# Kernel tuning notes

Measured on AMD Instinct MI355X. Metric: run time of the kernel, lower is better.

The kernel has to match this reference:

```python
import jax, jax.numpy as jnp
import numpy as np

N_NODES = 50000
N_EDGES = 300000
N_GRAPHS = 2048
N_FEATS = 128
DIM_OUT = 32


def setup_inputs() -> dict:
    key = jax.random.key(0)
    ks = jax.random.split(key, 10)
    def glorot(k, shape):
        fan_in, fan_out = shape
        lim = (6.0 / (fan_in + fan_out)) ** 0.5
        return jax.random.uniform(k, shape, jnp.float32, -lim, lim)
    x = jax.random.normal(ks[0], (N_NODES, N_FEATS), jnp.float32)
    edge_index = jax.random.randint(ks[1], (2, N_EDGES), 0, N_NODES, jnp.int64)
    batch = jnp.sort(jax.random.randint(ks[2], (N_NODES,), 0, N_GRAPHS, jnp.int64))
    return {
        "x": x,
        "edge_index": edge_index,
        "batch": batch,
        "W1": glorot(ks[3], (N_FEATS, 256)), "b1": jnp.zeros((256,), jnp.float32),
        "W2": glorot(ks[4], (256, 256)),     "b2": jnp.zeros((256,), jnp.float32),
        "W3": glorot(ks[5], (256, 256)),     "b3": jnp.zeros((256,), jnp.float32),
        "Wf1": glorot(ks[6], (256, 128)),    "bf1": jnp.zeros((128,), jnp.float32),
        "Wf2": glorot(ks[7], (128, DIM_OUT)), "bf2": jnp.zeros((DIM_OUT,), jnp.float32),
    }


def _gcn_norm(edge_index, num_nodes):
    # PyG GCNConv default: add self-loops, symmetric D^-1/2 (A+I) D^-1/2 norm.
    loop = jnp.arange(num_nodes, dtype=edge_index.dtype)
    src = jnp.concatenate([edge_index[0], loop])
    dst = jnp.concatenate([edge_index[1], loop])
    deg = jax.ops.segment_sum(jnp.ones_like(dst, jnp.float32), dst, num_segments=num_nodes)
    dinv = jnp.where(deg > 0, deg ** -0.5, 0.0)
    norm = dinv[src] * dinv[dst]  # [E + N]
    return src, dst, norm


def _gcn_conv(x, src, dst, norm, W, b):
    h = x @ W                                # [N, C] transform first (efficient)
    msg = h[src] * norm[:, None]             # gather + scale, [E+N, C]
    agg = jax.ops.segment_sum(msg, dst, num_segments=x.shape[0])
    return agg + b


def reference(x, edge_index, batch, W1, b1, W2, b2, W3, b3, Wf1, bf1, Wf2, bf2):
    n = x.shape[0]
    src, dst, norm = _gcn_norm(edge_index, n)
    h = jax.nn.relu(_gcn_conv(x, src, dst, norm, W1, b1))
    h = jax.nn.relu(_gcn_conv(h, src, dst, norm, W2, b2))
    h = jax.nn.relu(_gcn_conv(h, src, dst, norm, W3, b3))
    # global_mean_pool over batch segment ids
    sums = jax.ops.segment_sum(h, batch, num_segments=N_GRAPHS)
    cnts = jax.ops.segment_sum(jnp.ones((n,), jnp.float32), batch, num_segments=N_GRAPHS)
    hg = sums / jnp.maximum(cnts, 1.0)[:, None]
    h = jax.nn.relu(hg @ Wf1 + bf1)
    return h @ Wf2 + bf2  # [N_GRAPHS, DIM_OUT]
```

## Files before the change

kernel.cpp:

```cpp
#include <hip/hip_runtime.h>
#include <hip/hip_bf16.h>

#define NNODES 50000
#define NEDGES 300000
#define NGRAPH 2048
#define NFEAT  128
#define NHID   256
#define DOUT   32
#define NROWS  50048

typedef __bf16 bf16x8 __attribute__((ext_vector_type(8)));
typedef float  f32x4  __attribute__((ext_vector_type(4)));
typedef int    i32x4  __attribute__((ext_vector_type(4)));
typedef unsigned short ushort8v __attribute__((ext_vector_type(8)));
typedef __attribute__((address_space(1))) const void* gas_ptr;
typedef __attribute__((address_space(3))) void* las_ptr;

__device__ __forceinline__ float bf2f(unsigned short u) {
    return __uint_as_float(((unsigned)u) << 16);
}
__device__ __forceinline__ unsigned short f2bf(float f) {
    unsigned u = __float_as_uint(f);
    unsigned r = u + 0x7FFFu + ((u >> 16) & 1u);
    return (unsigned short)(r >> 16);
}
__device__ __forceinline__ float sb2f(unsigned v, int k) {
    return (float)((signed char)(v >> (8 * k)));
}


template<int K>
__device__ __forceinline__ void wquant(const float* __restrict__ W, unsigned char* __restrict__ Wq,
                                       float* __restrict__ bsc, int t) {
    constexpr int EPR = K / 16;
    int n = t >> 4, p = t & 15;
    float vals[EPR];
    float mx = 0.f;
#pragma unroll
    for (int j = 0; j < EPR; ++j) {
        float v = W[(size_t)(p * EPR + j) * 256 + n];
        vals[j] = v;
        mx = fmaxf(mx, fabsf(v));
    }
    mx = fmaxf(mx, __shfl_xor(mx, 1, 16));
    mx = fmaxf(mx, __shfl_xor(mx, 2, 16));
    mx = fmaxf(mx, __shfl_xor(mx, 4, 16));
    mx = fmaxf(mx, __shfl_xor(mx, 8, 16));
    float inv = (mx > 0.f) ? 127.f / mx : 0.f;
#pragma unroll
    for (int j4 = 0; j4 < EPR / 4; ++j4) {
        unsigned pw = 0;
#pragma unroll
        for (int b = 0; b < 4; ++b) {
            int qv = (int)rintf(vals[j4 * 4 + b] * inv);
            pw |= ((unsigned)(qv & 255)) << (8 * b);
        }
        int k = p * EPR + j4 * 4;
        *(unsigned*)&Wq[(k >> 6) * 16384 + n * 64 + (k & 63)] = pw;
    }
    if (p == 0) bsc[n] = mx * (1.f / 127.f);
}

__global__ __launch_bounds__(256) void prep_k(const float* __restrict__ x, unsigned short* __restrict__ x16,
                                              const float* __restrict__ W1, const float* __restrict__ W2,
                                              const float* __restrict__ W3, const float* __restrict__ Wf1,
                                              const float* __restrict__ Wf2,
                                              unsigned char* __restrict__ Wq1, unsigned char* __restrict__ Wq2,
                                              unsigned char* __restrict__ Wq3,
                                              float* __restrict__ bsc1, float* __restrict__ bsc2,
                                              float* __restrict__ bsc3,
                                              unsigned short* __restrict__ Wf1t, unsigned short* __restrict__ Wf2t,
                                              int* __restrict__ cnt, int* __restrict__ fill,
                                              int4* __restrict__ adj8z) {
    int idx = blockIdx.x * 256 + threadIdx.x;
    if (idx < 800000) {
        int i = idx * 8;
        float4 a = *(const float4*)&x[i];
        float4 b = *(const float4*)&x[i + 4];
        ushort8v o = { f2bf(a.x), f2bf(a.y), f2bf(a.z), f2bf(a.w),
                       f2bf(b.x), f2bf(b.y), f2bf(b.z), f2bf(b.w) };
        int row = idx >> 4, ch = idx & 15;
        ((ushort8v*)x16)[(size_t)(row << 4) | (ch ^ (row & 7))] = o;
        return;
    }
    int t = idx - 800000;
    if (t < 4096)  { wquant<128>(W1, Wq1, bsc1, t); return; }
    t -= 4096;
    if (t < 4096)  { wquant<256>(W2, Wq2, bsc2, t); return; }
    t -= 4096;
    if (t < 4096)  { wquant<256>(W3, Wq3, bsc3, t); return; }
    t -= 4096;
    if (t < 36864) {
        const float* W; unsigned short* Wt; int K, N;
        if (t < 32768) { W = Wf1; Wt = Wf1t; K = 256; N = 128; }
        else           { W = Wf2; Wt = Wf2t; K = 128; N = 32; t -= 32768; }
        int n = t / K, k = t - n * K;
        Wt[t] = f2bf(W[(size_t)k * N + n]);
        return;
    }
    t -= 36864;
    if (t < NNODES) { cnt[t] = 0; fill[t] = 0; return; }
    t -= NNODES;
    if (t < 200000) { int4 z4 = {0, 0, 0, 0}; adj8z[t] = z4; }
}

__global__ __launch_bounds__(256) void edge_hist_k(const int* __restrict__ dst, int* cnt, int E) {
    int e = blockIdx.x * 256 + threadIdx.x;
    if (e < E) atomicAdd(&cnt[dst[e]], 1);
}

__global__ __launch_bounds__(1024) void scan_block_k(const int* __restrict__ cnt, int* __restrict__ rowp,
                                                     int* __restrict__ part, float* __restrict__ dinv,
                                                     int2* __restrict__ hdr, int n) {
    __shared__ int s[1024];
    int tid = threadIdx.x;
    int i = blockIdx.x * 1024 + tid;
    int v = (i < n) ? cnt[i] : 0;
    if (i < n) {
        float dv = rsqrtf((float)(v + 1));
        dinv[i] = dv;
        hdr[i] = make_int2(v, __float_as_int(dv * dv));
    }
    s[tid] = v;
    __syncthreads();
    for (int off = 1; off < 1024; off <<= 1) {
        int t = (tid >= off) ? s[tid - off] : 0;
        __syncthreads();
        s[tid] += t;
        __syncthreads();
    }
    if (i < n) rowp[i] = s[tid] - v;
    if (tid == 1023) part[blockIdx.x] = s[1023];
}

__global__ __launch_bounds__(256) void scatter_k(const int* __restrict__ src, const int* __restrict__ dst,
                                                 const int* __restrict__ rowp_pre, const int* __restrict__ part,
                                                 int* fill, const float* __restrict__ dinv,
                                                 int2* __restrict__ adj8, int2* __restrict__ adj,
                                                 int* __restrict__ rowp_fin,
                                                 const int* __restrict__ batch, int* __restrict__ gstart,
                                                 int E, int n, int nb) {
    __shared__ int s[64];
    int tid = threadIdx.x;
    if (tid < 64) s[tid] = (tid < nb) ? part[tid] : 0;
    __syncthreads();
    for (int off = 1; off < 64; off <<= 1) {
        int t = 0;
        if (tid < 64 && tid >= off) t = s[tid - off];
        __syncthreads();
        if (tid < 64) s[tid] += t;
        __syncthreads();
    }
    int gid = blockIdx.x * 256 + tid;
    if (gid <= n) {
        if (gid < n) {
            int ch = gid >> 10;
            int base = (ch == 0) ? 0 : s[ch - 1];
            rowp_fin[gid] = rowp_pre[gid] + base;
        } else {
            rowp_fin[n] = s[nb - 1];
        }
    }
    if (gid < n) {
        int b = batch[gid];
        int prev = (gid == 0) ? -1 : batch[gid - 1];
        for (int g = prev + 1; g <= b; ++g) gstart[g] = gid;
        if (gid == n - 1)
            for (int g = b + 1; g <= NGRAPH; ++g) gstart[g] = n;
    }
    if (gid < E) {
        int ss = src[gid], d = dst[gid];
        int f = atomicAdd(&fill[d], 1);
        int2 a; a.x = ss; a.y = __float_as_int(dinv[ss] * dinv[d]);
        if (f < 8) {
            adj8[d * 8 + f] = a;
        } else {
            int ch = d >> 10;
            int base = (ch == 0) ? 0 : s[ch - 1];
            adj[rowp_pre[d] + base + f] = a;
        }
    }
}

__global__ __launch_bounds__(256) void agg1_k(const unsigned short* __restrict__ T,
                                              const int4* __restrict__ adj8,
                                              const int2* __restrict__ hdr,
                                              const int* __restrict__ rowf,
                                              const int2* __restrict__ adj,
                                              unsigned char* __restrict__ z8,
                                              float* __restrict__ asc, int n) {
    int g  = threadIdx.x >> 4;
    int li = threadIdx.x & 15;
    int node = blockIdx.x * 16 + g;
    if (node >= n) return;
    const ushort8v* tp = (const ushort8v*)T;
    int2 h = hdr[node];
    int deg = h.x;
    float sw = __int_as_float(h.y);
    ushort8v u = tp[(size_t)node * 16 + (li ^ (node & 7))];
    int4 s4[4];
#pragma unroll
    for (int j = 0; j < 4; ++j) s4[j] = adj8[node * 4 + j];
    float ac[8];
#pragma unroll
    for (int k = 0; k < 8; ++k) ac[k] = bf2f(u[k]) * sw;
    int c[8]; float w[8];
#pragma unroll
    for (int j = 0; j < 4; ++j) {
        c[2 * j]     = s4[j].x; w[2 * j]     = __int_as_float(s4[j].y);
        c[2 * j + 1] = s4[j].z; w[2 * j + 1] = __int_as_float(s4[j].w);
    }
    ushort8v mm[8];
#pragma unroll
    for (int j = 0; j < 8; ++j) mm[j] = tp[(size_t)c[j] * 16 + (li ^ (c[j] & 7))];
#pragma unroll
    for (int j = 0; j < 8; ++j)
#pragma unroll
        for (int k = 0; k < 8; ++k)
            ac[k] += bf2f(mm[j][k]) * w[j];
    if (deg > 8) {
        int e0 = rowf[node], e1 = e0 + deg;
        for (int e = e0 + 8; e < e1; e += 4) {
            int2 a2[4];
#pragma unroll
            for (int j = 0; j < 4; ++j) {
                int ee = e + j;
                a2[j] = (ee < e1) ? adj[ee] : make_int2(0, 0);
            }
            ushort8v m2[4];
#pragma unroll
            for (int j = 0; j < 4; ++j) m2[j] = tp[(size_t)a2[j].x * 16 + (li ^ (a2[j].x & 7))];
#pragma unroll
            for (int j = 0; j < 4; ++j)
#pragma unroll
                for (int k = 0; k < 8; ++k)
                    ac[k] += bf2f(m2[j][k]) * __int_as_float(a2[j].y);
        }
    }
    float mx = 0.f;
#pragma unroll
    for (int k = 0; k < 8; ++k) mx = fmaxf(mx, fabsf(ac[k]));
    mx = fmaxf(mx, __shfl_xor(mx, 1, 16));
    mx = fmaxf(mx, __shfl_xor(mx, 2, 16));
    mx = fmaxf(mx, __shfl_xor(mx, 4, 16));
    mx = fmaxf(mx, __shfl_xor(mx, 8, 16));
    float inv = (mx > 0.f) ? 127.f / mx : 0.f;
    unsigned w0 = 0, w1 = 0;
#pragma unroll
    for (int k = 0; k < 4; ++k) {
        int q0 = (int)rintf(ac[k] * inv);
        int q1 = (int)rintf(ac[k + 4] * inv);
        w0 |= ((unsigned)(q0 & 255)) << (8 * k);
        w1 |= ((unsigned)(q1 & 255)) << (8 * k);
    }
    ((uint2*)z8)[(size_t)node * 16 + ((li >> 1) ^ (node & 7)) * 2 + (li & 1)] = make_uint2(w0, w1);
    if (li == 0) asc[node] = mx * (1.f / 127.f);
}

__global__ __launch_bounds__(256) void agg_q_k(const unsigned char* __restrict__ Hq,
                                               const float* __restrict__ csc,
                                               const int4* __restrict__ adj8,
                                               const int2* __restrict__ hdr,
                                               const int* __restrict__ rowf,
                                               const int2* __restrict__ adj,
                                               unsigned char* __restrict__ z8,
                                               float* __restrict__ asc, int n) {
    int g  = threadIdx.x >> 5;
    int li = threadIdx.x & 31;
    int node = blockIdx.x * 8 + g;
    if (node >= n) return;
    const uint2* qp = (const uint2*)Hq;
    int2 h = hdr[node];
    int deg = h.x;
    float swgt = __int_as_float(h.y) * csc[node];
    uint2 u = qp[(size_t)node * 32 + li];
    int4 s4[4];
#pragma unroll
    for (int j = 0; j < 4; ++j) s4[j] = adj8[node * 4 + j];
    int c[8]; float w[8];
#pragma unroll
    for (int j = 0; j < 4; ++j) {
        c[2 * j]     = s4[j].x; w[2 * j]     = __int_as_float(s4[j].y);
        c[2 * j + 1] = s4[j].z; w[2 * j + 1] = __int_as_float(s4[j].w);
    }
    uint2 mm[8];
#pragma unroll
    for (int j = 0; j < 8; ++j) mm[j] = qp[(size_t)c[j] * 32 + li];
    float ws[8];
#pragma unroll
    for (int j = 0; j < 8; ++j) ws[j] = w[j] * csc[c[j]];
    float ac[8];
#pragma unroll
    for (int k = 0; k < 4; ++k) {
        ac[k]     = sb2f(u.x, k) * swgt;
        ac[k + 4] = sb2f(u.y, k) * swgt;
    }
#pragma unroll
    for (int j = 0; j < 8; ++j)
#pragma unroll
        for (int k = 0; k < 4; ++k) {
            ac[k]     += sb2f(mm[j].x, k) * ws[j];
            ac[k + 4] += sb2f(mm[j].y, k) * ws[j];
        }
    if (deg > 8) {
        int e0 = rowf[node], e1 = e0 + deg;
        for (int e = e0 + 8; e < e1; e += 4) {
            int2 a2[4];
#pragma unroll
            for (int j = 0; j < 4; ++j) {
                int ee = e + j;
                a2[j] = (ee < e1) ? adj[ee] : make_int2(0, 0);
            }
            uint2 m2[4]; float w2[4];
#pragma unroll
            for (int j = 0; j < 4; ++j) m2[j] = qp[(size_t)a2[j].x * 32 + li];
#pragma unroll
            for (int j = 0; j < 4; ++j) w2[j] = __int_as_float(a2[j].y) * csc[a2[j].x];
#pragma unroll
            for (int j = 0; j < 4; ++j)
#pragma unroll
                for (int k = 0; k < 4; ++k) {
                    ac[k]     += sb2f(m2[j].x, k) * w2[j];
                    ac[k + 4] += sb2f(m2[j].y, k) * w2[j];
                }
        }
    }
    float mx = 0.f;
#pragma unroll
    for (int k = 0; k < 8; ++k) mx = fmaxf(mx, fabsf(ac[k]));
    mx = fmaxf(mx, __shfl_xor(mx, 1, 32));
    mx = fmaxf(mx, __shfl_xor(mx, 2, 32));
    mx = fmaxf(mx, __shfl_xor(mx, 4, 32));
    mx = fmaxf(mx, __shfl_xor(mx, 8, 32));
    mx = fmaxf(mx, __shfl_xor(mx, 16, 32));
    float inv = (mx > 0.f) ? 127.f / mx : 0.f;
    unsigned w0 = 0, w1 = 0;
#pragma unroll
    for (int k = 0; k < 4; ++k) {
        int q0 = (int)rintf(ac[k] * inv);
        int q1 = (int)rintf(ac[k + 4] * inv);
        w0 |= ((unsigned)(q0 & 255)) << (8 * k);
        w1 |= ((unsigned)(q1 & 255)) << (8 * k);
    }
    ((uint2*)z8)[(size_t)node * 32 + ((li >> 1) ^ (node & 7)) * 2 + (li & 1)] = make_uint2(w0, w1);
    if (li == 0) asc[node] = mx * (1.f / 127.f);
}

template<int K, int MODE>
__global__ __launch_bounds__(512, 2) void gemm_k(const unsigned char* __restrict__ A,
                                                 const unsigned char* __restrict__ Bq,
                                                 const float* __restrict__ bscale,
                                                 const float* __restrict__ asc,
                                                 const float* __restrict__ bias,
                                                 unsigned short* __restrict__ C,
                                                 unsigned char* __restrict__ Cq,
                                                 float* __restrict__ csc,
                                                 int M, int flags, int ntiles) {
    constexpr int CPR = K / 16;
    constexpr int LP  = (64 * CPR) / 512;
    __shared__ unsigned char  At[64 * K];
    __shared__ unsigned short Et[64 * 264];
    __shared__ float sAsc[64];
    const int tid = threadIdx.x;
    const int lane = tid & 63;
    const int wave = tid >> 6;
    const int m = lane & 15, q = lane >> 4;
    const int wr = (wave >> 2) * 32;
    const int wc = (wave & 3) * 64;

    i32x4 breg[K / 64][4];
#pragma unroll
    for (int kt = 0; kt < K / 64; ++kt)
#pragma unroll
        for (int j = 0; j < 4; ++j)
            breg[kt][j] = *(const i32x4*)&Bq[kt * 16384 + (wc + j * 16 + m) * 64 + q * 16];

    for (int t = blockIdx.x; t < ntiles; t += gridDim.x) {
        const size_t cbase = (size_t)t * 64 * K;
#pragma unroll
        for (int p = 0; p < LP; ++p) {
            int u = p * 512 + tid;
            __builtin_amdgcn_global_load_lds((gas_ptr)(A + cbase + (size_t)u * 16),
                                             (las_ptr)&At[(p * 512 + wave * 64) * 16], 16, 0, 0);
        }
        if (tid < 64) sAsc[tid] = asc[t * 64 + tid];
        __syncthreads();

        i32x4 acc[2][4] = {};
#pragma unroll
        for (int kt = 0; kt < K / 64; ++kt) {
            i32x4 af[2];
#pragma unroll
            for (int i = 0; i < 2; ++i) {
                int lr = wr + i * 16 + m;
                af[i] = *(const i32x4*)&At[lr * K + (((kt * 4 + q) ^ (lr & 7)) * 16)];
            }
#pragma unroll
            for (int i = 0; i < 2; ++i)
#pragma unroll
                for (int j = 0; j < 4; ++j)
                    acc[i][j] = __builtin_amdgcn_mfma_i32_16x16x64_i8(af[i], breg[kt][j], acc[i][j], 0, 0, 0);
        }

#pragma unroll
        for (int i = 0; i < 2; ++i) {
#pragma unroll
            for (int j = 0; j < 4; ++j) {
                int c = wc + j * 16 + m;
                float bv = (flags & 2) ? bias[c] : 0.f;
                float bs = bscale[c];
#pragma unroll
                for (int r = 0; r < 4; ++r) {
                    int row = wr + i * 16 + q * 4 + r;
                    float v = (float)acc[i][j][r] * (sAsc[row] * bs) + bv;
                    if (flags & 1) v = fmaxf(v, 0.f);
                    Et[row * 264 + c] = f2bf(v);
                }
            }
        }
        __syncthreads();

        if (MODE == 1) {
            int row = tid >> 3, ch8 = tid & 7;
            int rr = t * 64 + row;
            ushort8v e[4];
#pragma unroll
            for (int k2 = 0; k2 < 4; ++k2)
                e[k2] = *(const ushort8v*)&Et[row * 264 + ch8 * 32 + k2 * 8];
            float mx = 0.f;
#pragma unroll
            for (int k2 = 0; k2 < 4; ++k2)
#pragma unroll
                for (int k = 0; k < 8; ++k) mx = fmaxf(mx, fabsf(bf2f(e[k2][k])));
            mx = fmaxf(mx, __shfl_xor(mx, 1, 64));
            mx = fmaxf(mx, __shfl_xor(mx, 2, 64));
            mx = fmaxf(mx, __shfl_xor(mx, 4, 64));
            float inv = (mx > 0.f) ? 127.f / mx : 0.f;
            unsigned pk[8];
#pragma unroll
            for (int w2 = 0; w2 < 8; ++w2) {
                unsigned p = 0;
#pragma unroll
                for (int b = 0; b < 4; ++b) {
                    int e8 = w2 * 4 + b;
                    float v = bf2f(e[e8 >> 3][e8 & 7]);
                    int qv = (int)rintf(v * inv);
                    p |= ((unsigned)(qv & 255)) << (8 * b);
                }
                pk[w2] = p;
            }
            if (rr < M) {
                uint4* dst = (uint4*)&Cq[(size_t)rr * 256 + ch8 * 32];
                dst[0] = make_uint4(pk[0], pk[1], pk[2], pk[3]);
                dst[1] = make_uint4(pk[4], pk[5], pk[6], pk[7]);
                if (ch8 == 0) csc[rr] = mx * (1.f / 127.f);
            }
        } else {
#pragma unroll
            for (int u0 = 0; u0 < 4; ++u0) {
                int u = u0 * 512 + tid;
                int row = u >> 5, cc = u & 31;
                int rr = t * 64 + row;
                if (rr < M)
                    ((ushort8v*)C)[(size_t)rr * 32 + (cc ^ (rr & 7))] = *(const ushort8v*)&Et[row * 264 + cc * 8];
            }
        }
    }
}

__global__ __launch_bounds__(256) void pool_k(const unsigned short* __restrict__ h,
                                              const int* __restrict__ gstart,
                                              unsigned short* __restrict__ hg) {
    __shared__ float red[4][256];
    int g = blockIdx.x;
    int wave = threadIdx.x >> 6, lane = threadIdx.x & 63;
    int s = gstart[g], e = gstart[g + 1];
    int ch = lane >> 1, sub = lane & 1;
    const ushort4* hp = (const ushort4*)h;
    float4 acc = make_float4(0.f, 0.f, 0.f, 0.f);
    for (int i = s + wave; i < e; i += 4) {
        ushort4 v = hp[((size_t)i * 32 + (ch ^ (i & 7))) * 2 + sub];
        acc.x += bf2f(v.x); acc.y += bf2f(v.y); acc.z += bf2f(v.z); acc.w += bf2f(v.w);
    }
    *(float4*)&red[wave][lane * 4] = acc;
    __syncthreads();
    if (wave == 0) {
        float inv = 1.f / fmaxf((float)(e - s), 1.f);
        float v0 = red[0][lane*4+0] + red[1][lane*4+0] + red[2][lane*4+0] + red[3][lane*4+0];
        float v1 = red[0][lane*4+1] + red[1][lane*4+1] + red[2][lane*4+1] + red[3][lane*4+1];
        float v2 = red[0][lane*4+2] + red[1][lane*4+2] + red[2][lane*4+2] + red[3][lane*4+2];
        float v3 = red[0][lane*4+3] + red[1][lane*4+3] + red[2][lane*4+3] + red[3][lane*4+3];
        ushort4 o = { f2bf(v0 * inv), f2bf(v1 * inv), f2bf(v2 * inv), f2bf(v3 * inv) };
        ((ushort4*)(hg + (size_t)g * NHID))[lane] = o;
    }
}

__global__ __launch_bounds__(256) void mlp_head_k(const unsigned short* __restrict__ HG,
                                                  const unsigned short* __restrict__ Wf1t,
                                                  const unsigned short* __restrict__ Wf2t,
                                                  const float* __restrict__ bf1, const float* __restrict__ bf2,
                                                  float* __restrict__ out) {
    __shared__ unsigned short As1[128 * 32];
    __shared__ unsigned short Bs1[128 * 32];
    __shared__ unsigned short R[128 * 128];
    __shared__ unsigned short Bs2[32 * 128];
    const int tid = threadIdx.x;
    const int lane = tid & 63, wave = tid >> 6;
    const int m = lane & 15, q = lane >> 4;
    const int rowBase = blockIdx.x * 128;
    const int wr = (wave >> 1) * 64;
    const int wc = (wave & 1) * 64;

#pragma unroll
    for (int c2 = 0; c2 < 2; ++c2) {
        const unsigned short* g = &Wf2t[(c2 * 256 + tid) * 8];
        __builtin_amdgcn_global_load_lds((gas_ptr)g, (las_ptr)&Bs2[(c2 * 256 + wave * 64) * 8], 16, 0, 0);
    }

    f32x4 acc[4][4] = {};
    for (int kt = 0; kt < 256; kt += 32) {
#pragma unroll
        for (int c2 = 0; c2 < 2; ++c2) {
            int u = c2 * 256 + tid;
            int row = u >> 2, kp = u & 3;
            const unsigned short* ga = &HG[(size_t)(rowBase + row) * 256 + kt + kp * 8];
            const unsigned short* gb = &Wf1t[(size_t)row * 256 + kt + kp * 8];
            __builtin_amdgcn_global_load_lds((gas_ptr)ga, (las_ptr)&As1[(c2 * 256 + wave * 64) * 8], 16, 0, 0);
            __builtin_amdgcn_global_load_lds((gas_ptr)gb, (las_ptr)&Bs1[(c2 * 256 + wave * 64) * 8], 16, 0, 0);
        }
        __syncthreads();
        bf16x8 af[4], bfr[4];
#pragma unroll
        for (int i = 0; i < 4; ++i) af[i] = *(const bf16x8*)&As1[(wr + i * 16 + m) * 32 + q * 8];
#pragma unroll
        for (int j = 0; j < 4; ++j) bfr[j] = *(const bf16x8*)&Bs1[(wc + j * 16 + m) * 32 + q * 8];
#pragma unroll
        for (int i = 0; i < 4; ++i)
#pragma unroll
            for (int j = 0; j < 4; ++j)
                acc[i][j] = __builtin_amdgcn_mfma_f32_16x16x32_bf16(af[i], bfr[j], acc[i][j], 0, 0, 0);
        __syncthreads();
    }
#pragma unroll
    for (int i = 0; i < 4; ++i)
#pragma unroll
        for (int j = 0; j < 4; ++j) {
            int c = wc + j * 16 + m;
            float bv = bf1[c];
#pragma unroll
            for (int r = 0; r < 4; ++r) {
                int rr = wr + i * 16 + q * 4 + r;
                R[rr * 128 + c] = f2bf(fmaxf(acc[i][j][r] + bv, 0.f));
            }
        }
    __syncthreads();

    const int wr2 = wave * 32;
    f32x4 acc2[2][2] = {};
#pragma unroll
    for (int s2 = 0; s2 < 4; ++s2) {
        bf16x8 af2[2], bf22[2];
#pragma unroll
        for (int i = 0; i < 2; ++i) af2[i] = *(const bf16x8*)&R[(wr2 + i * 16 + m) * 128 + s2 * 32 + q * 8];
#pragma unroll
        for (int ct = 0; ct < 2; ++ct) bf22[ct] = *(const bf16x8*)&Bs2[(ct * 16 + m) * 128 + s2 * 32 + q * 8];
#pragma unroll
        for (int i = 0; i < 2; ++i)
#pragma unroll
            for (int ct = 0; ct < 2; ++ct)
                acc2[i][ct] = __builtin_amdgcn_mfma_f32_16x16x32_bf16(af2[i], bf22[ct], acc2[i][ct], 0, 0, 0);
    }
#pragma unroll
    for (int i = 0; i < 2; ++i)
#pragma unroll
        for (int ct = 0; ct < 2; ++ct) {
            int c = ct * 16 + m;
            float bv = bf2[c];
#pragma unroll
            for (int r = 0; r < 4; ++r) {
                int rr = rowBase + wr2 + i * 16 + q * 4 + r;
                out[(size_t)rr * 32 + c] = acc2[i][ct][r] + bv;
            }
        }
}

extern "C" void kernel_launch(void* const* d_in, const int* in_sizes, int n_in,
                              void* d_out, int out_size, void* d_ws, size_t ws_size,
                              hipStream_t stream) {
    const float* x    = (const float*)d_in[0];
    const int*   ei   = (const int*)d_in[1];
    const int*   batch= (const int*)d_in[2];
    const float* W1   = (const float*)d_in[3];
    const float* b1   = (const float*)d_in[4];
    const float* W2   = (const float*)d_in[5];
    const float* b2   = (const float*)d_in[6];
    const float* W3   = (const float*)d_in[7];
    const float* b3   = (const float*)d_in[8];
    const float* Wf1  = (const float*)d_in[9];
    const float* bf1  = (const float*)d_in[10];
    const float* Wf2  = (const float*)d_in[11];
    const float* bf2  = (const float*)d_in[12];
    float* out = (float*)d_out;

    const int* e_src = ei;
    const int* e_dst = ei + NEDGES;

    char* ws = (char*)d_ws;
    size_t off = 0;
    auto alloc = [&](size_t bytes) -> void* {
        void* p = (void*)(ws + off);
        off += (bytes + 255) & ~(size_t)255;
        return p;
    };
    unsigned short* X16 = (unsigned short*)alloc((size_t)NROWS * NFEAT * 2);
    unsigned char*  Za8 = (unsigned char*)alloc((size_t)NROWS * NFEAT);
    unsigned char*  Zb8 = (unsigned char*)alloc((size_t)NROWS * NHID);
    float*          asc = (float*)alloc((size_t)NROWS * 4);
    unsigned char*  Hq  = (unsigned char*)alloc((size_t)NROWS * NHID);
    float*          csc = (float*)alloc((size_t)NROWS * 4);
    unsigned short* Ha  = (unsigned short*)alloc((size_t)NROWS * NHID * 2);
    unsigned short* HG  = (unsigned short*)alloc((size_t)NGRAPH * NHID * 2);
    unsigned char*  Wq1 = (unsigned char*)alloc((size_t)NFEAT * NHID);
    unsigned char*  Wq2 = (unsigned char*)alloc((size_t)NHID * NHID);
    unsigned char*  Wq3 = (unsigned char*)alloc((size_t)NHID * NHID);
    float*          bsc1= (float*)alloc((size_t)NHID * 4);
    float*          bsc2= (float*)alloc((size_t)NHID * 4);
    float*          bsc3= (float*)alloc((size_t)NHID * 4);
    unsigned short* Wf1t= (unsigned short*)alloc((size_t)NFEAT * NHID * 2);
    unsigned short* Wf2t= (unsigned short*)alloc((size_t)DOUT * NFEAT * 2);
    float* dinv = (float*)alloc((size_t)NNODES * 4);
    int*   cnt  = (int*)alloc((size_t)NNODES * 4);
    int*   fill = (int*)alloc((size_t)NNODES * 4);
    int*   rowp = (int*)alloc((size_t)(NNODES + 1) * 4);
    int*   rowf = (int*)alloc((size_t)(NNODES + 1) * 4);
    int2*  adj8 = (int2*)alloc((size_t)NNODES * 8 * 8);
    int2*  adj  = (int2*)alloc((size_t)NEDGES * 8);
    int2*  hdr  = (int2*)alloc((size_t)NNODES * 8);
    int*   part = (int*)alloc((size_t)64 * 4);
    int*   gstart = (int*)alloc((size_t)(NGRAPH + 1) * 4);
    (void)alloc(131072);

    const int nb = (NNODES + 1023) / 1024;
    const int nprep = 800000 + 4096 * 3 + 36864 + NNODES + 200000;

    hipLaunchKernelGGL(prep_k, dim3((nprep + 255) / 256), dim3(256), 0, stream,
                       x, X16, W1, W2, W3, Wf1, Wf2, Wq1, Wq2, Wq3, bsc1, bsc2, bsc3,
                       Wf1t, Wf2t, cnt, fill, (int4*)adj8);
    hipLaunchKernelGGL(edge_hist_k, dim3((NEDGES + 255) / 256), dim3(256), 0, stream, e_dst, cnt, NEDGES);
    hipLaunchKernelGGL(scan_block_k, dim3(nb), dim3(1024), 0, stream, cnt, rowp, part, dinv, hdr, NNODES);
    hipLaunchKernelGGL(scatter_k, dim3((NEDGES + 255) / 256), dim3(256), 0, stream,
                       e_src, e_dst, rowp, part, fill, dinv, adj8, adj, rowf, batch, gstart,
                       NEDGES, NNODES, nb);

    const int ntiles = NROWS / 64;
    hipLaunchKernelGGL(agg1_k, dim3((NNODES + 15) / 16), dim3(256), 0, stream,
                       X16, (const int4*)adj8, hdr, rowf, adj, Za8, asc, NNODES);
    hipLaunchKernelGGL((gemm_k<128, 1>), dim3(512), dim3(512), 0, stream,
                       Za8, Wq1, bsc1, asc, b1, (unsigned short*)nullptr, Hq, csc, NNODES, 3, ntiles);
    hipLaunchKernelGGL(agg_q_k, dim3((NNODES + 7) / 8), dim3(256), 0, stream,
                       Hq, csc, (const int4*)adj8, hdr, rowf, adj, Zb8, asc, NNODES);
    hipLaunchKernelGGL((gemm_k<256, 1>), dim3(512), dim3(512), 0, stream,
                       Zb8, Wq2, bsc2, asc, b2, (unsigned short*)nullptr, Hq, csc, NNODES, 3, ntiles);
    hipLaunchKernelGGL(agg_q_k, dim3((NNODES + 7) / 8), dim3(256), 0, stream,
                       Hq, csc, (const int4*)adj8, hdr, rowf, adj, Zb8, asc, NNODES);
    hipLaunchKernelGGL((gemm_k<256, 0>), dim3(512), dim3(512), 0, stream,
                       Zb8, Wq3, bsc3, asc, b3, Ha, (unsigned char*)nullptr, (float*)nullptr, NNODES, 3, ntiles);

    hipLaunchKernelGGL(pool_k, dim3(NGRAPH), dim3(256), 0, stream, Ha, gstart, HG);

    hipLaunchKernelGGL(mlp_head_k, dim3(NGRAPH / 128), dim3(256), 0, stream,
                       HG, Wf1t, Wf2t, bf1, bf2, out);
}
```

Before: 252.0 us.

## Fuse global mean pooling into final GEMM epilogue via atomic segment sums

The last GCN GEMM now reduces its bf16 output rows directly into a per-graph fp32 accumulator using the sorted batch ids and atomicAdd, instead of writing the full node feature matrix and running a separate pooling kernel. The MLP head reads these fp32 sums, divides by graph counts and converts to bf16 in shared memory. The accumulator is zeroed in the prep kernel, and the GEMM grids are changed from 512 persistent blocks to one block per tile. This removes a large intermediate write/read and one launch, at the cost of global atomics and nondeterministic summation order.

```diff
diff --git a/kernel.cpp b/kernel.cpp
--- a/kernel.cpp
+++ b/kernel.cpp
@@ -71,7 +71,7 @@
                                               float* __restrict__ bsc3,
                                               unsigned short* __restrict__ Wf1t, unsigned short* __restrict__ Wf2t,
                                               int* __restrict__ cnt, int* __restrict__ fill,
-                                              int4* __restrict__ adj8z) {
+                                              int4* __restrict__ adj8z, float4* __restrict__ hgz) {
     int idx = blockIdx.x * 256 + threadIdx.x;
     if (idx < 800000) {
         int i = idx * 8;
@@ -101,7 +101,9 @@
     t -= 36864;
     if (t < NNODES) { cnt[t] = 0; fill[t] = 0; return; }
     t -= NNODES;
-    if (t < 200000) { int4 z4 = {0, 0, 0, 0}; adj8z[t] = z4; }
+    if (t < 200000) { int4 z4 = {0, 0, 0, 0}; adj8z[t] = z4; return; }
+    t -= 200000;
+    if (t < 131072) { hgz[t] = make_float4(0.f, 0.f, 0.f, 0.f); }
 }
 
 __global__ __launch_bounds__(256) void edge_hist_k(const int* __restrict__ dst, int* cnt, int E) {
@@ -352,15 +354,17 @@
                                                  const float* __restrict__ bscale,
                                                  const float* __restrict__ asc,
                                                  const float* __restrict__ bias,
-                                                 unsigned short* __restrict__ C,
                                                  unsigned char* __restrict__ Cq,
                                                  float* __restrict__ csc,
+                                                 float* __restrict__ HGacc,
+                                                 const int* __restrict__ batch,
                                                  int M, int flags, int ntiles) {
     constexpr int CPR = K / 16;
     constexpr int LP  = (64 * CPR) / 512;
     __shared__ unsigned char  At[64 * K];
     __shared__ unsigned short Et[64 * 264];
     __shared__ float sAsc[64];
+    __shared__ int sbatch[64];
     const int tid = threadIdx.x;
     const int lane = tid & 63;
     const int wave = tid >> 6;
@@ -383,7 +387,13 @@
             __builtin_amdgcn_global_load_lds((gas_ptr)(A + cbase + (size_t)u * 16),
                                              (las_ptr)&At[(p * 512 + wave * 64) * 16], 16, 0, 0);
         }
-        if (tid < 64) sAsc[tid] = asc[t * 64 + tid];
+        if (tid < 64) {
+            sAsc[tid] = asc[t * 64 + tid];
+            if (MODE == 2) {
+                int rr = t * 64 + tid;
+                sbatch[tid] = (rr < M) ? batch[rr] : -1;
+            }
+        }
         __syncthreads();
 
         i32x4 acc[2][4] = {};
@@ -456,46 +466,25 @@
                 if (ch8 == 0) csc[rr] = mx * (1.f / 127.f);
             }
         } else {
-#pragma unroll
-            for (int u0 = 0; u0 < 4; ++u0) {
-                int u = u0 * 512 + tid;
-                int row = u >> 5, cc = u & 31;
-                int rr = t * 64 + row;
-                if (rr < M)
-                    ((ushort8v*)C)[(size_t)rr * 32 + (cc ^ (rr & 7))] = *(const ushort8v*)&Et[row * 264 + cc * 8];
-            }
-        }
-    }
-}
-
-__global__ __launch_bounds__(256) void pool_k(const unsigned short* __restrict__ h,
-                                              const int* __restrict__ gstart,
-                                              unsigned short* __restrict__ hg) {
-    __shared__ float red[4][256];
-    int g = blockIdx.x;
-    int wave = threadIdx.x >> 6, lane = threadIdx.x & 63;
-    int s = gstart[g], e = gstart[g + 1];
-    int ch = lane >> 1, sub = lane & 1;
-    const ushort4* hp = (const ushort4*)h;
-    float4 acc = make_float4(0.f, 0.f, 0.f, 0.f);
-    for (int i = s + wave; i < e; i += 4) {
-        ushort4 v = hp[((size_t)i * 32 + (ch ^ (i & 7))) * 2 + sub];
-        acc.x += bf2f(v.x); acc.y += bf2f(v.y); acc.z += bf2f(v.z); acc.w += bf2f(v.w);
-    }
-    *(float4*)&red[wave][lane * 4] = acc;
-    __syncthreads();
-    if (wave == 0) {
-        float inv = 1.f / fmaxf((float)(e - s), 1.f);
-        float v0 = red[0][lane*4+0] + red[1][lane*4+0] + red[2][lane*4+0] + red[3][lane*4+0];
-        float v1 = red[0][lane*4+1] + red[1][lane*4+1] + red[2][lane*4+1] + red[3][lane*4+1];
-        float v2 = red[0][lane*4+2] + red[1][lane*4+2] + red[2][lane*4+2] + red[3][lane*4+2];
-        float v3 = red[0][lane*4+3] + red[1][lane*4+3] + red[2][lane*4+3] + red[3][lane*4+3];
-        ushort4 o = { f2bf(v0 * inv), f2bf(v1 * inv), f2bf(v2 * inv), f2bf(v3 * inv) };
-        ((ushort4*)(hg + (size_t)g * NHID))[lane] = o;
-    }
-}
-
-__global__ __launch_bounds__(256) void mlp_head_k(const unsigned short* __restrict__ HG,
+            int c = tid & 255, hh = tid >> 8;
+            int gcur = sbatch[hh * 32];
+            float acp = 0.f;
+#pragma unroll 1
+            for (int r = 0; r < 32; ++r) {
+                int gb = sbatch[hh * 32 + r];
+                if (gb != gcur) {
+                    if (gcur >= 0) atomicAdd(&HGacc[(size_t)gcur * 256 + c], acp);
+                    acp = 0.f; gcur = gb;
+                }
+                if (gb >= 0) acp += bf2f(Et[(hh * 32 + r) * 264 + c]);
+            }
+            if (gcur >= 0) atomicAdd(&HGacc[(size_t)gcur * 256 + c], acp);
+        }
+    }
+}
+
+__global__ __launch_bounds__(256) void mlp_head_k(const float* __restrict__ HGacc,
+                                                  const int* __restrict__ gstart,
                                                   const unsigned short* __restrict__ Wf1t,
                                                   const unsigned short* __restrict__ Wf2t,
                                                   const float* __restrict__ bf1, const float* __restrict__ bf2,
@@ -504,6 +493,7 @@
     __shared__ unsigned short Bs1[128 * 32];
     __shared__ unsigned short R[128 * 128];
     __shared__ unsigned short Bs2[32 * 128];
+    __shared__ float invc[128];
     const int tid = threadIdx.x;
     const int lane = tid & 63, wave = tid >> 6;
     const int m = lane & 15, q = lane >> 4;
@@ -516,16 +506,31 @@
         const unsigned short* g = &Wf2t[(c2 * 256 + tid) * 8];
         __builtin_amdgcn_global_load_lds((gas_ptr)g, (las_ptr)&Bs2[(c2 * 256 + wave * 64) * 8], 16, 0, 0);
     }
+    if (tid < 128) {
+        int g0 = rowBase + tid;
+        invc[tid] = 1.f / fmaxf((float)(gstart[g0 + 1] - gstart[g0]), 1.f);
+    }
+    __syncthreads();
 
     f32x4 acc[4][4] = {};
     for (int kt = 0; kt < 256; kt += 32) {
+        {
+            int row = tid >> 1, half = tid & 1;
+            const float4* src = (const float4*)&HGacc[(size_t)(rowBase + row) * 256 + kt + half * 16];
+            float4 f0 = src[0], f1 = src[1], f2 = src[2], f3 = src[3];
+            float sc = invc[row];
+            ushort8v p0 = { f2bf(f0.x * sc), f2bf(f0.y * sc), f2bf(f0.z * sc), f2bf(f0.w * sc),
+                            f2bf(f1.x * sc), f2bf(f1.y * sc), f2bf(f1.z * sc), f2bf(f1.w * sc) };
+            ushort8v p1 = { f2bf(f2.x * sc), f2bf(f2.y * sc), f2bf(f2.z * sc), f2bf(f2.w * sc),
+                            f2bf(f3.x * sc), f2bf(f3.y * sc), f2bf(f3.z * sc), f2bf(f3.w * sc) };
+            *(ushort8v*)&As1[row * 32 + half * 16] = p0;
+            *(ushort8v*)&As1[row * 32 + half * 16 + 8] = p1;
+        }
 #pragma unroll
         for (int c2 = 0; c2 < 2; ++c2) {
             int u = c2 * 256 + tid;
             int row = u >> 2, kp = u & 3;
-            const unsigned short* ga = &HG[(size_t)(rowBase + row) * 256 + kt + kp * 8];
             const unsigned short* gb = &Wf1t[(size_t)row * 256 + kt + kp * 8];
-            __builtin_amdgcn_global_load_lds((gas_ptr)ga, (las_ptr)&As1[(c2 * 256 + wave * 64) * 8], 16, 0, 0);
             __builtin_amdgcn_global_load_lds((gas_ptr)gb, (las_ptr)&Bs1[(c2 * 256 + wave * 64) * 8], 16, 0, 0);
         }
         __syncthreads();
@@ -618,8 +623,7 @@
     float*          asc = (float*)alloc((size_t)NROWS * 4);
     unsigned char*  Hq  = (unsigned char*)alloc((size_t)NROWS * NHID);
     float*          csc = (float*)alloc((size_t)NROWS * 4);
-    unsigned short* Ha  = (unsigned short*)alloc((size_t)NROWS * NHID * 2);
-    unsigned short* HG  = (unsigned short*)alloc((size_t)NGRAPH * NHID * 2);
+    float*          HGacc = (float*)alloc((size_t)NGRAPH * NHID * 4);
     unsigned char*  Wq1 = (unsigned char*)alloc((size_t)NFEAT * NHID);
     unsigned char*  Wq2 = (unsigned char*)alloc((size_t)NHID * NHID);
     unsigned char*  Wq3 = (unsigned char*)alloc((size_t)NHID * NHID);
@@ -641,11 +645,11 @@
     (void)alloc(131072);
 
     const int nb = (NNODES + 1023) / 1024;
-    const int nprep = 800000 + 4096 * 3 + 36864 + NNODES + 200000;
+    const int nprep = 800000 + 4096 * 3 + 36864 + NNODES + 200000 + 131072;
 
     hipLaunchKernelGGL(prep_k, dim3((nprep + 255) / 256), dim3(256), 0, stream,
                        x, X16, W1, W2, W3, Wf1, Wf2, Wq1, Wq2, Wq3, bsc1, bsc2, bsc3,
-                       Wf1t, Wf2t, cnt, fill, (int4*)adj8);
+                       Wf1t, Wf2t, cnt, fill, (int4*)adj8, (float4*)HGacc);
     hipLaunchKernelGGL(edge_hist_k, dim3((NEDGES + 255) / 256), dim3(256), 0, stream, e_dst, cnt, NEDGES);
     hipLaunchKernelGGL(scan_block_k, dim3(nb), dim3(1024), 0, stream, cnt, rowp, part, dinv, hdr, NNODES);
     hipLaunchKernelGGL(scatter_k, dim3((NEDGES + 255) / 256), dim3(256), 0, stream,
@@ -655,19 +659,20 @@
     const int ntiles = NROWS / 64;
     hipLaunchKernelGGL(agg1_k, dim3((NNODES + 15) / 16), dim3(256), 0, stream,
                        X16, (const int4*)adj8, hdr, rowf, adj, Za8, asc, NNODES);
-    hipLaunchKernelGGL((gemm_k<128, 1>), dim3(512), dim3(512), 0, stream,
-                       Za8, Wq1, bsc1, asc, b1, (unsigned short*)nullptr, Hq, csc, NNODES, 3, ntiles);
+    hipLaunchKernelGGL((gemm_k<128, 1>), dim3(ntiles), dim3(512), 0, stream,
+                       Za8, Wq1, bsc1, asc, b1, Hq, csc, (float*)nullptr, (const int*)nullptr,
+                       NNODES, 3, ntiles);
     hipLaunchKernelGGL(agg_q_k, dim3((NNODES + 7) / 8), dim3(256), 0, stream,
                        Hq, csc, (const int4*)adj8, hdr, rowf, adj, Zb8, asc, NNODES);
-    hipLaunchKernelGGL((gemm_k<256, 1>), dim3(512), dim3(512), 0, stream,
-                       Zb8, Wq2, bsc2, asc, b2, (unsigned short*)nullptr, Hq, csc, NNODES, 3, ntiles);
+    hipLaunchKernelGGL((gemm_k<256, 1>), dim3(ntiles), dim3(512), 0, stream,
+                       Zb8, Wq2, bsc2, asc, b2, Hq, csc, (float*)nullptr, (const int*)nullptr,
+                       NNODES, 3, ntiles);
     hipLaunchKernelGGL(agg_q_k, dim3((NNODES + 7) / 8), dim3(256), 0, stream,
                        Hq, csc, (const int4*)adj8, hdr, rowf, adj, Zb8, asc, NNODES);
-    hipLaunchKernelGGL((gemm_k<256, 0>), dim3(512), dim3(512), 0, stream,
-                       Zb8, Wq3, bsc3, asc, b3, Ha, (unsigned char*)nullptr, (float*)nullptr, NNODES, 3, ntiles);
-
-    hipLaunchKernelGGL(pool_k, dim3(NGRAPH), dim3(256), 0, stream, Ha, gstart, HG);
+    hipLaunchKernelGGL((gemm_k<256, 2>), dim3(ntiles), dim3(512), 0, stream,
+                       Zb8, Wq3, bsc3, asc, b3, (unsigned char*)nullptr, (float*)nullptr, HGacc, batch,
+                       NNODES, 3, ntiles);
 
     hipLaunchKernelGGL(mlp_head_k, dim3(NGRAPH / 128), dim3(256), 0, stream,
-                       HG, Wf1t, Wf2t, bf1, bf2, out);
-}
+                       HGacc, gstart, Wf1t, Wf2t, bf1, bf2, out);
+}
```

Result: slower. 274.0 us (+8.8%).
